# Kernel tuning notes

Measured on AMD Instinct MI355X. Metric: run time of the kernel, lower is better.

Reference implementation:

```python
import jax, jax.numpy as jnp
import numpy as np

WSCALE = 0.05  # keep ReLU MLP activations in a sane range


def setup_inputs() -> dict:
    key = jax.random.key(0)
    ks = jax.random.split(key, 9)
    B, D, H = 2048, 64, 512
    return {
        "x": jax.random.normal(ks[0], (B, D), dtype=jnp.float32),
        "W1": jax.random.normal(ks[1], (H, D), dtype=jnp.float32) * WSCALE,
        "b1": jax.random.normal(ks[2], (H,), dtype=jnp.float32) * WSCALE,
        "W2": jax.random.normal(ks[3], (H, H), dtype=jnp.float32) * WSCALE,
        "b2": jax.random.normal(ks[4], (H,), dtype=jnp.float32) * WSCALE,
        "W3": jax.random.normal(ks[5], (H, H), dtype=jnp.float32) * WSCALE,
        "b3": jax.random.normal(ks[6], (H,), dtype=jnp.float32) * WSCALE,
        "W4": jax.random.normal(ks[7], (D, H), dtype=jnp.float32) * WSCALE,
        "b4": jax.random.normal(ks[8], (D,), dtype=jnp.float32) * WSCALE,
    }


def reference(x, W1, b1, W2, b2, W3, b3, W4, b4):
    # Score network: ReLU MLP (weights stored PyTorch-style [out, in]).
    a1 = x @ W1.T + b1          # [B, H]
    h1 = jax.nn.relu(a1)
    a2 = h1 @ W2.T + b2
    h2 = jax.nn.relu(a2)
    a3 = h2 @ W3.T + b3
    h3 = jax.nn.relu(a3)
    s = h3 @ W4.T + b4          # [B, D] score

    # Divergence = trace of Jacobian ds/dx per sample.
    # Per-sample J = W4 @ diag(m3) @ W3 @ diag(m2) @ W2 @ diag(m1) @ W1,
    # with m_k = 1[a_k > 0] (ReLU derivative; 0 at 0 like torch autograd).
    m1 = (a1 > 0).astype(x.dtype)
    m2 = (a2 > 0).astype(x.dtype)
    m3 = (a3 > 0).astype(x.dtype)
    T = m1[:, :, None] * W1[None, :, :]                 # [B, H, D]
    T = m2[:, :, None] * jnp.einsum('ij,bjd->bid', W2, T)  # [B, H, D]
    T = m3[:, :, None] * jnp.einsum('ij,bjd->bid', W3, T)  # [B, H, D]
    div = jnp.einsum('dj,bjd->b', W4, T)                # trace of J, [B]

    # Hyvarinen score: 0.5 * ||s||^2 + div
    val = 0.5 * jnp.sum(s * s, axis=1) + div
    return val
```

## Files before the change

### kernel.cpp

```cpp
#include <hip/hip_runtime.h>
#include <stdint.h>


typedef __attribute__((ext_vector_type(8))) short short8;
typedef __attribute__((ext_vector_type(4))) float f32x4;

union U16x8 {
  uint4 u;
  short8 s;
};

__device__ __forceinline__ uint16_t f2bf(float f) {
  uint32_t u = __float_as_uint(f);
  uint32_t lsb = (u >> 16) & 1u;
  u += 0x7FFFu + lsb;
  return (uint16_t)(u >> 16);
}

__global__ __launch_bounds__(256) void convert_kernel(
    const float* __restrict__ W1, const float* __restrict__ W2,
    const float* __restrict__ W3, const float* __restrict__ W4,
    uint16_t* __restrict__ A2swz, uint16_t* __restrict__ A3swz,
    uint16_t* __restrict__ B1swz, uint16_t* __restrict__ B4swz,
    float* __restrict__ W2Tf, float* __restrict__ W3Tf,
    float* __restrict__ W1Tf, float* __restrict__ W4Tf) {
  const int i = blockIdx.x * 256 + threadIdx.x;
  if (i < 262144) {
    const int e = i;
    const int f = e >> 3, j = e & 7;
    const int lane = f & 63, fk = f >> 6;
    const int kc = fk & 15, r16 = fk >> 4;
    const int l15 = lane & 15, quad = lane >> 4;
    const int row = r16 * 16 + l15, col = kc * 32 + quad * 8 + j;
    A2swz[e] = f2bf(W2[row * 512 + col]);
  } else if (i < 524288) {
    const int e = i - 262144;
    const int f = e >> 3, j = e & 7;
    const int lane = f & 63, fk = f >> 6;
    const int kc = fk & 15, r16 = fk >> 4;
    const int l15 = lane & 15, quad = lane >> 4;
    const int row = r16 * 16 + l15, col = kc * 32 + quad * 8 + j;
    A3swz[e] = f2bf(W3[col * 512 + row]);
  } else if (i < 557056) {
    const int e = i - 524288;
    const int f = e >> 3, j = e & 7;
    const int lane = f & 63, fk = f >> 6;
    const int kc = fk >> 2, jt = fk & 3;
    const int l15 = lane & 15, quad = lane >> 4;
    const int d = jt * 16 + l15, col = kc * 32 + quad * 8 + j;
    B1swz[e] = f2bf(W1[col * 64 + d]);
  } else if (i < 589824) {
    const int e = i - 557056;
    const int f = e >> 3, j = e & 7;
    const int lane = f & 63, fk = f >> 6;
    const int kc = fk >> 2, jt = fk & 3;
    const int l15 = lane & 15, quad = lane >> 4;
    const int d = jt * 16 + l15, col = kc * 32 + quad * 8 + j;
    B4swz[e] = f2bf(W4[d * 512 + col]);
  } else if (i < 851968) {
    const int e = i - 589824;
    const int k = e >> 9, jj = e & 511;
    W2Tf[e] = W2[jj * 512 + k];
  } else if (i < 1114112) {
    const int e = i - 851968;
    const int k = e >> 9, jj = e & 511;
    W3Tf[e] = W3[jj * 512 + k];
  } else if (i < 1146880) {
    const int e = i - 1114112;
    const int k = e >> 9, jj = e & 511;
    W1Tf[e] = W1[jj * 64 + k];
  } else if (i < 1179648) {
    const int e = i - 1146880;
    const int k = e >> 6, d = e & 63;
    W4Tf[e] = W4[d * 512 + k];
  }
}

__device__ __forceinline__ void fwd_hidden(
    const float* __restrict__ WT, const float* __restrict__ bias,
    const float2* __restrict__ src,
    float2* __restrict__ dst,
    uint32_t* __restrict__ mw, uint32_t* __restrict__ mglob,
    int sh, int jq, int t, int K) {
  const int j4 = jq * 4;
  float a[4][2];
  {
    const float4 bb = *(const float4*)(bias + j4);
    a[0][0] = bb.x; a[0][1] = bb.x;
    a[1][0] = bb.y; a[1][1] = bb.y;
    a[2][0] = bb.z; a[2][1] = bb.z;
    a[3][0] = bb.w; a[3][1] = bb.w;
  }
#pragma unroll 8
  for (int k = 0; k < K; ++k) {
    const float4 w = *(const float4*)(WT + (size_t)k * 512 + j4);
    const float2 h = src[k * 2];
    a[0][0] = fmaf(w.x, h.x, a[0][0]); a[0][1] = fmaf(w.x, h.y, a[0][1]);
    a[1][0] = fmaf(w.y, h.x, a[1][0]); a[1][1] = fmaf(w.y, h.y, a[1][1]);
    a[2][0] = fmaf(w.z, h.x, a[2][0]); a[2][1] = fmaf(w.z, h.y, a[2][1]);
    a[3][0] = fmaf(w.w, h.x, a[3][0]); a[3][1] = fmaf(w.w, h.y, a[3][1]);
  }
  const int word = jq >> 3, shift = 4 * (jq & 7);
#pragma unroll
  for (int si = 0; si < 2; ++si) {
    uint32_t nib = (a[0][si] > 0.f ? 1u : 0u) | (a[1][si] > 0.f ? 2u : 0u) |
                   (a[2][si] > 0.f ? 4u : 0u) | (a[3][si] > 0.f ? 8u : 0u);
    if (nib) atomicOr(&mw[(sh * 2 + si) * 16 + word], nib << shift);
  }
#pragma unroll
  for (int u = 0; u < 4; ++u) {
    float2 r;
    r.x = a[u][0] > 0.f ? a[u][0] : 0.f;
    r.y = a[u][1] > 0.f ? a[u][1] : 0.f;
    dst[(j4 + u) * 2] = r;
  }
  __syncthreads();
  if (t < 128) {
    mglob[(size_t)(t >> 4) * 16 + (t & 15)] = mw[t];
    mw[t] = 0;
  }
  __syncthreads();
}

__global__ __launch_bounds__(512) void forward_kernel(
    const float* __restrict__ x,
    const float* __restrict__ W1Tf, const float* __restrict__ b1,
    const float* __restrict__ W2Tf, const float* __restrict__ b2,
    const float* __restrict__ W3Tf, const float* __restrict__ b3,
    const float* __restrict__ W4Tf, const float* __restrict__ b4,
    uint32_t* __restrict__ m1p, uint32_t* __restrict__ m2p,
    uint32_t* __restrict__ m3p, float* __restrict__ out) {
  __shared__ float4 xs[2][64];
  __shared__ float4 hp[2][2][512];
  __shared__ uint32_t mw[128];
  const int t = threadIdx.x;
  const int b0 = blockIdx.x * 8;
  const int sh = t >> 7;
  const int jq = t & 127;
  const int g = sh >> 1;
  const int half = sh & 1;

  {
    const int k = t >> 3, s = t & 7;
    ((float*)&xs[s >> 2][k])[s & 3] = x[(size_t)(b0 + s) * 64 + k];
    if (t < 128) mw[t] = 0;
  }
  __syncthreads();

  fwd_hidden(W1Tf, b1, (const float2*)&xs[g][0] + half,
             (float2*)&hp[0][g][0] + half, mw, m1p + (size_t)b0 * 16, sh, jq, t, 64);
  fwd_hidden(W2Tf, b2, (const float2*)&hp[0][g][0] + half,
             (float2*)&hp[1][g][0] + half, mw, m2p + (size_t)b0 * 16, sh, jq, t, 512);
  fwd_hidden(W3Tf, b3, (const float2*)&hp[1][g][0] + half,
             (float2*)&hp[0][g][0] + half, mw, m3p + (size_t)b0 * 16, sh, jq, t, 512);

  {
    const int wv = t >> 6, lane = t & 63;
    const int s = wv;
    const float* h = (const float*)&hp[0][s >> 2][0] + (s & 3);
    float acc = b4[lane];
#pragma unroll 8
    for (int k = 0; k < 512; ++k)
      acc = fmaf(W4Tf[k * 64 + lane], h[k * 4], acc);
    float sq = acc * acc;
#pragma unroll
    for (int off = 32; off; off >>= 1) sq += __shfl_down(sq, off, 64);
    if (lane == 0) out[b0 + s] = 0.5f * sq;
  }
}

__device__ __forceinline__ void expand_mask(uint32_t byte8, uint32_t mk[4]) {
#pragma unroll
  for (int i = 0; i < 4; ++i) {
    mk[i] = (((byte8 >> (2 * i)) & 1u) ? 0x0000FFFFu : 0u) |
            (((byte8 >> (2 * i + 1)) & 1u) ? 0xFFFF0000u : 0u);
  }
}

__global__ __launch_bounds__(256, 2) void div_kernel(
    const uint4* __restrict__ A2swz, const uint4* __restrict__ A3swz,
    const uint4* __restrict__ B1swz, const uint4* __restrict__ B4swz,
    const uint32_t* __restrict__ m1p, const uint32_t* __restrict__ m2p,
    const uint32_t* __restrict__ m3p, float* __restrict__ out) {
  const int t = threadIdx.x;
  const int lane = t & 63, wv = t >> 6;
  const int sLoc = wv & 1, rh = wv >> 1;
  const int l15 = lane & 15, quad = lane >> 4;
  const int g = blockIdx.x;
  const int rowB0 = blockIdx.y * 128;
  const int b = g * 2 + sLoc;
  const int r16b = (rowB0 >> 4) + rh * 4;

  f32x4 accC[4][4], accG[4][4];
#pragma unroll
  for (int it = 0; it < 4; ++it)
#pragma unroll
    for (int jt = 0; jt < 4; ++jt) {
      accC[it][jt] = (f32x4){0.f, 0.f, 0.f, 0.f};
      accG[it][jt] = (f32x4){0.f, 0.f, 0.f, 0.f};
    }

  const uint32_t* m1w = m1p + (size_t)b * 16;
  const uint32_t* m3w = m3p + (size_t)b * 16;

#pragma unroll 1
  for (int kc = 0; kc < 16; ++kc) {
    uint4 a2[4], u1[4], a3[4], u4[4];
#pragma unroll
    for (int it = 0; it < 4; ++it)
      a2[it] = A2swz[(size_t)((r16b + it) * 16 + kc) * 64 + lane];
#pragma unroll
    for (int jt = 0; jt < 4; ++jt)
      u1[jt] = B1swz[(size_t)(kc * 4 + jt) * 64 + lane];
#pragma unroll
    for (int it = 0; it < 4; ++it)
      a3[it] = A3swz[(size_t)((r16b + it) * 16 + kc) * 64 + lane];
#pragma unroll
    for (int jt = 0; jt < 4; ++jt)
      u4[jt] = B4swz[(size_t)(kc * 4 + jt) * 64 + lane];

    const uint32_t m1d = __builtin_amdgcn_readfirstlane(m1w[kc]);
    const uint32_t m3d = __builtin_amdgcn_readfirstlane(m3w[kc]);
    uint32_t mk1[4], mk3[4];
    expand_mask((m1d >> (quad * 8)) & 0xFFu, mk1);
    expand_mask((m3d >> (quad * 8)) & 0xFFu, mk3);

    short8 bC[4];
#pragma unroll
    for (int jt = 0; jt < 4; ++jt) {
      U16x8 u;
      u.u = u1[jt];
      u.u.x &= mk1[0]; u.u.y &= mk1[1]; u.u.z &= mk1[2]; u.u.w &= mk1[3];
      bC[jt] = u.s;
    }
#pragma unroll
    for (int it = 0; it < 4; ++it) {
      U16x8 ua;
      ua.u = a2[it];
      const short8 af = ua.s;
#pragma unroll
      for (int jt = 0; jt < 4; ++jt)
        accC[it][jt] = __builtin_amdgcn_mfma_f32_16x16x32_bf16(af, bC[jt], accC[it][jt], 0, 0, 0);
    }
    short8 bG[4];
#pragma unroll
    for (int jt = 0; jt < 4; ++jt) {
      U16x8 u;
      u.u = u4[jt];
      u.u.x &= mk3[0]; u.u.y &= mk3[1]; u.u.z &= mk3[2]; u.u.w &= mk3[3];
      bG[jt] = u.s;
    }
#pragma unroll
    for (int it = 0; it < 4; ++it) {
      U16x8 ua;
      ua.u = a3[it];
      const short8 af = ua.s;
#pragma unroll
      for (int jt = 0; jt < 4; ++jt)
        accG[it][jt] = __builtin_amdgcn_mfma_f32_16x16x32_bf16(af, bG[jt], accG[it][jt], 0, 0, 0);
    }
  }

  const uint32_t* m2w = m2p + (size_t)b * 16;
  float dsum = 0.f;
#pragma unroll
  for (int it = 0; it < 4; ++it) {
    const int rloc = rh * 64 + it * 16 + quad * 4;
    const uint32_t md = m2w[(rowB0 + rloc) >> 5];
    const uint32_t bits = (md >> (rloc & 31)) & 0xFu;
    const float w0 = (bits & 1u) ? 1.f : 0.f;
    const float w1 = (bits & 2u) ? 1.f : 0.f;
    const float w2 = (bits & 4u) ? 1.f : 0.f;
    const float w3 = (bits & 8u) ? 1.f : 0.f;
#pragma unroll
    for (int jt = 0; jt < 4; ++jt) {
      dsum = fmaf(w0, accC[it][jt][0] * accG[it][jt][0], dsum);
      dsum = fmaf(w1, accC[it][jt][1] * accG[it][jt][1], dsum);
      dsum = fmaf(w2, accC[it][jt][2] * accG[it][jt][2], dsum);
      dsum = fmaf(w3, accC[it][jt][3] * accG[it][jt][3], dsum);
    }
  }
#pragma unroll
  for (int off = 32; off; off >>= 1) dsum += __shfl_down(dsum, off, 64);
  if (lane == 0) atomicAdd(out + b, dsum);
}

extern "C" void kernel_launch(void* const* d_in, const int* in_sizes, int n_in,
                              void* d_out, int out_size, void* d_ws, size_t ws_size,
                              hipStream_t stream) {
  const float* x  = (const float*)d_in[0];
  const float* W1 = (const float*)d_in[1];
  const float* b1 = (const float*)d_in[2];
  const float* W2 = (const float*)d_in[3];
  const float* b2 = (const float*)d_in[4];
  const float* W3 = (const float*)d_in[5];
  const float* b3 = (const float*)d_in[6];
  const float* W4 = (const float*)d_in[7];
  const float* b4 = (const float*)d_in[8];
  float* out = (float*)d_out;

  char* ws = (char*)d_ws;
  uint16_t* A2swz = (uint16_t*)(ws + 0);
  uint16_t* A3swz = (uint16_t*)(ws + 524288);
  uint16_t* B1swz = (uint16_t*)(ws + 1048576);
  uint16_t* B4swz = (uint16_t*)(ws + 1114112);
  float*    W2Tf  = (float*)(ws + 1179648);
  float*    W3Tf  = (float*)(ws + 2228224);
  float*    W1Tf  = (float*)(ws + 3276800);
  float*    W4Tf  = (float*)(ws + 3407872);
  uint32_t* m1p   = (uint32_t*)(ws + 3538944);
  uint32_t* m2p   = (uint32_t*)(ws + 3670016);
  uint32_t* m3p   = (uint32_t*)(ws + 3801088);
  if (ws_size < 3932160) return;

  convert_kernel<<<4608, 256, 0, stream>>>(W1, W2, W3, W4,
                                           A2swz, A3swz, B1swz, B4swz,
                                           W2Tf, W3Tf, W1Tf, W4Tf);
  forward_kernel<<<256, 512, 0, stream>>>(x, W1Tf, b1, W2Tf, b2, W3Tf, b3,
                                          W4Tf, b4, m1p, m2p, m3p, out);
  div_kernel<<<dim3(1024, 4), 256, 0, stream>>>((const uint4*)A2swz,
                                                (const uint4*)A3swz,
                                                (const uint4*)B1swz,
                                                (const uint4*)B4swz,
                                                m1p, m2p, m3p, out);
}
```

Before: 297.2 us.

## Share divergence fragments via LDS across four samples and widen forward blocks

The divergence kernel now has each block handle four samples over 64 rows. Its bf16 weight fragments are staged once per block into double-buffered LDS with global_load_lds, and all four waves reuse them instead of each wave loading its own copy from global memory. The forward kernel moves to 1024-thread blocks, with each thread computing two hidden units instead of four, to raise parallelism. The costs are extra LDS, a block barrier every k-chunk, and more atomicOr contention on the mask words.

```diff
diff --git a/kernel.cpp b/kernel.cpp
--- a/kernel.cpp
+++ b/kernel.cpp
@@ -15,6 +15,12 @@
   uint32_t lsb = (u >> 16) & 1u;
   u += 0x7FFFu + lsb;
   return (uint16_t)(u >> 16);
+}
+
+__device__ __forceinline__ void lds_load16(const uint4* gsrc, uint4* ldst) {
+  __builtin_amdgcn_global_load_lds(
+      (const __attribute__((address_space(1))) void*)gsrc,
+      (__attribute__((address_space(3))) void*)ldst, 16, 0, 0);
 }
 
 __global__ __launch_bounds__(256) void convert_kernel(
@@ -81,38 +87,33 @@
     const float2* __restrict__ src,
     float2* __restrict__ dst,
     uint32_t* __restrict__ mw, uint32_t* __restrict__ mglob,
-    int sh, int jq, int t, int K) {
-  const int j4 = jq * 4;
-  float a[4][2];
+    int sh, int jq2, int t, int K) {
+  const int j2 = jq2 * 2;
+  float a[2][2];
   {
-    const float4 bb = *(const float4*)(bias + j4);
+    const float2 bb = *(const float2*)(bias + j2);
     a[0][0] = bb.x; a[0][1] = bb.x;
     a[1][0] = bb.y; a[1][1] = bb.y;
-    a[2][0] = bb.z; a[2][1] = bb.z;
-    a[3][0] = bb.w; a[3][1] = bb.w;
   }
 #pragma unroll 8
   for (int k = 0; k < K; ++k) {
-    const float4 w = *(const float4*)(WT + (size_t)k * 512 + j4);
+    const float2 w = *(const float2*)(WT + (size_t)k * 512 + j2);
     const float2 h = src[k * 2];
     a[0][0] = fmaf(w.x, h.x, a[0][0]); a[0][1] = fmaf(w.x, h.y, a[0][1]);
     a[1][0] = fmaf(w.y, h.x, a[1][0]); a[1][1] = fmaf(w.y, h.y, a[1][1]);
-    a[2][0] = fmaf(w.z, h.x, a[2][0]); a[2][1] = fmaf(w.z, h.y, a[2][1]);
-    a[3][0] = fmaf(w.w, h.x, a[3][0]); a[3][1] = fmaf(w.w, h.y, a[3][1]);
-  }
-  const int word = jq >> 3, shift = 4 * (jq & 7);
+  }
+  const int word = jq2 >> 4, shift = 2 * (jq2 & 15);
 #pragma unroll
   for (int si = 0; si < 2; ++si) {
-    uint32_t nib = (a[0][si] > 0.f ? 1u : 0u) | (a[1][si] > 0.f ? 2u : 0u) |
-                   (a[2][si] > 0.f ? 4u : 0u) | (a[3][si] > 0.f ? 8u : 0u);
+    uint32_t nib = (a[0][si] > 0.f ? 1u : 0u) | (a[1][si] > 0.f ? 2u : 0u);
     if (nib) atomicOr(&mw[(sh * 2 + si) * 16 + word], nib << shift);
   }
 #pragma unroll
-  for (int u = 0; u < 4; ++u) {
+  for (int u = 0; u < 2; ++u) {
     float2 r;
     r.x = a[u][0] > 0.f ? a[u][0] : 0.f;
     r.y = a[u][1] > 0.f ? a[u][1] : 0.f;
-    dst[(j4 + u) * 2] = r;
+    dst[(j2 + u) * 2] = r;
   }
   __syncthreads();
   if (t < 128) {
@@ -122,7 +123,7 @@
   __syncthreads();
 }
 
-__global__ __launch_bounds__(512) void forward_kernel(
+__global__ __launch_bounds__(1024) void forward_kernel(
     const float* __restrict__ x,
     const float* __restrict__ W1Tf, const float* __restrict__ b1,
     const float* __restrict__ W2Tf, const float* __restrict__ b2,
@@ -135,37 +136,39 @@
   __shared__ uint32_t mw[128];
   const int t = threadIdx.x;
   const int b0 = blockIdx.x * 8;
-  const int sh = t >> 7;
-  const int jq = t & 127;
+  const int sh = t >> 8;
+  const int jq2 = t & 255;
   const int g = sh >> 1;
   const int half = sh & 1;
 
-  {
+  if (t < 512) {
     const int k = t >> 3, s = t & 7;
     ((float*)&xs[s >> 2][k])[s & 3] = x[(size_t)(b0 + s) * 64 + k];
-    if (t < 128) mw[t] = 0;
-  }
+  }
+  if (t < 128) mw[t] = 0;
   __syncthreads();
 
   fwd_hidden(W1Tf, b1, (const float2*)&xs[g][0] + half,
-             (float2*)&hp[0][g][0] + half, mw, m1p + (size_t)b0 * 16, sh, jq, t, 64);
+             (float2*)&hp[0][g][0] + half, mw, m1p + (size_t)b0 * 16, sh, jq2, t, 64);
   fwd_hidden(W2Tf, b2, (const float2*)&hp[0][g][0] + half,
-             (float2*)&hp[1][g][0] + half, mw, m2p + (size_t)b0 * 16, sh, jq, t, 512);
+             (float2*)&hp[1][g][0] + half, mw, m2p + (size_t)b0 * 16, sh, jq2, t, 512);
   fwd_hidden(W3Tf, b3, (const float2*)&hp[1][g][0] + half,
-             (float2*)&hp[0][g][0] + half, mw, m3p + (size_t)b0 * 16, sh, jq, t, 512);
+             (float2*)&hp[0][g][0] + half, mw, m3p + (size_t)b0 * 16, sh, jq2, t, 512);
 
   {
     const int wv = t >> 6, lane = t & 63;
-    const int s = wv;
-    const float* h = (const float*)&hp[0][s >> 2][0] + (s & 3);
-    float acc = b4[lane];
+    if (wv < 8) {
+      const int s = wv;
+      const float* h = (const float*)&hp[0][s >> 2][0] + (s & 3);
+      float acc = b4[lane];
 #pragma unroll 8
-    for (int k = 0; k < 512; ++k)
-      acc = fmaf(W4Tf[k * 64 + lane], h[k * 4], acc);
-    float sq = acc * acc;
-#pragma unroll
-    for (int off = 32; off; off >>= 1) sq += __shfl_down(sq, off, 64);
-    if (lane == 0) out[b0 + s] = 0.5f * sq;
+      for (int k = 0; k < 512; ++k)
+        acc = fmaf(W4Tf[k * 64 + lane], h[k * 4], acc);
+      float sq = acc * acc;
+#pragma unroll
+      for (int off = 32; off; off >>= 1) sq += __shfl_down(sq, off, 64);
+      if (lane == 0) out[b0 + s] = 0.5f * sq;
+    }
   }
 }
 
@@ -182,14 +185,17 @@
     const uint4* __restrict__ B1swz, const uint4* __restrict__ B4swz,
     const uint32_t* __restrict__ m1p, const uint32_t* __restrict__ m2p,
     const uint32_t* __restrict__ m3p, float* __restrict__ out) {
+  __shared__ uint4 sfrag[2][16][64];
   const int t = threadIdx.x;
   const int lane = t & 63, wv = t >> 6;
-  const int sLoc = wv & 1, rh = wv >> 1;
   const int l15 = lane & 15, quad = lane >> 4;
-  const int g = blockIdx.x;
-  const int rowB0 = blockIdx.y * 128;
-  const int b = g * 2 + sLoc;
-  const int r16b = (rowB0 >> 4) + rh * 4;
+  (void)l15;
+  const int g4 = blockIdx.x;
+  const int rowB0 = blockIdx.y * 64;
+  const int b = g4 * 4 + wv;
+  const int r16b = blockIdx.y * 4;
+
+  const uint4* sb = (wv == 0) ? A2swz : (wv == 1) ? A3swz : (wv == 2) ? B1swz : B4swz;
 
   f32x4 accC[4][4], accG[4][4];
 #pragma unroll
@@ -203,21 +209,32 @@
   const uint32_t* m1w = m1p + (size_t)b * 16;
   const uint32_t* m3w = m3p + (size_t)b * 16;
 
+  auto stage = [&](int sbuf, int kc) {
+#pragma unroll
+    for (int q = 0; q < 4; ++q) {
+      const size_t off = (wv < 2)
+          ? ((size_t)((r16b + q) * 16 + kc) * 64 + lane)
+          : ((size_t)(kc * 4 + q) * 64 + lane);
+      lds_load16(sb + off, &sfrag[sbuf][wv * 4 + q][0]);
+    }
+  };
+
+  stage(0, 0);
+  __syncthreads();
+
+  int buf = 0;
 #pragma unroll 1
   for (int kc = 0; kc < 16; ++kc) {
-    uint4 a2[4], u1[4], a3[4], u4[4];
-#pragma unroll
-    for (int it = 0; it < 4; ++it)
-      a2[it] = A2swz[(size_t)((r16b + it) * 16 + kc) * 64 + lane];
-#pragma unroll
-    for (int jt = 0; jt < 4; ++jt)
-      u1[jt] = B1swz[(size_t)(kc * 4 + jt) * 64 + lane];
-#pragma unroll
-    for (int it = 0; it < 4; ++it)
-      a3[it] = A3swz[(size_t)((r16b + it) * 16 + kc) * 64 + lane];
-#pragma unroll
-    for (int jt = 0; jt < 4; ++jt)
-      u4[jt] = B4swz[(size_t)(kc * 4 + jt) * 64 + lane];
+    if (kc < 15) stage(buf ^ 1, kc + 1);
+
+    uint4 a2[4], a3[4], u1[4], u4[4];
+#pragma unroll
+    for (int q = 0; q < 4; ++q) {
+      a2[q] = sfrag[buf][q][lane];
+      a3[q] = sfrag[buf][4 + q][lane];
+      u1[q] = sfrag[buf][8 + q][lane];
+      u4[q] = sfrag[buf][12 + q][lane];
+    }
 
     const uint32_t m1d = __builtin_amdgcn_readfirstlane(m1w[kc]);
     const uint32_t m3d = __builtin_amdgcn_readfirstlane(m3w[kc]);
@@ -259,13 +276,15 @@
       for (int jt = 0; jt < 4; ++jt)
         accG[it][jt] = __builtin_amdgcn_mfma_f32_16x16x32_bf16(af, bG[jt], accG[it][jt], 0, 0, 0);
     }
+    __syncthreads();
+    buf ^= 1;
   }
 
   const uint32_t* m2w = m2p + (size_t)b * 16;
   float dsum = 0.f;
 #pragma unroll
   for (int it = 0; it < 4; ++it) {
-    const int rloc = rh * 64 + it * 16 + quad * 4;
+    const int rloc = it * 16 + quad * 4;
     const uint32_t md = m2w[(rowB0 + rloc) >> 5];
     const uint32_t bits = (md >> (rloc & 31)) & 0xFu;
     const float w0 = (bits & 1u) ? 1.f : 0.f;
@@ -316,11 +335,11 @@
   convert_kernel<<<4608, 256, 0, stream>>>(W1, W2, W3, W4,
                                            A2swz, A3swz, B1swz, B4swz,
                                            W2Tf, W3Tf, W1Tf, W4Tf);
-  forward_kernel<<<256, 512, 0, stream>>>(x, W1Tf, b1, W2Tf, b2, W3Tf, b3,
-                                          W4Tf, b4, m1p, m2p, m3p, out);
-  div_kernel<<<dim3(1024, 4), 256, 0, stream>>>((const uint4*)A2swz,
-                                                (const uint4*)A3swz,
-                                                (const uint4*)B1swz,
-                                                (const uint4*)B4swz,
-                                                m1p, m2p, m3p, out);
-}
+  forward_kernel<<<256, 1024, 0, stream>>>(x, W1Tf, b1, W2Tf, b2, W3Tf, b3,
+                                           W4Tf, b4, m1p, m2p, m3p, out);
+  div_kernel<<<dim3(512, 8), 256, 0, stream>>>((const uint4*)A2swz,
+                                               (const uint4*)A3swz,
+                                               (const uint4*)B1swz,
+                                               (const uint4*)B4swz,
+                                               m1p, m2p, m3p, out);
+}
```

New measurement: 355.4 us. +19.6%, slower.
